# Performance work log

Hardware: AMD Instinct MI355X
Metric: run time of the kernel (lower is better)

Reference implementation:

```python
import jax, jax.numpy as jnp
import numpy as np

N_FFT = 1024
HOP = 256
WIN_LEN = N_FFT  # win_length == n_fft
PAD = (WIN_LEN - HOP) // 2  # 'same' padding


def hann_window(n):
    # torch.hann_window default (periodic=True): 0.5*(1-cos(2*pi*k/n))
    k = jnp.arange(n, dtype=jnp.float32)
    return 0.5 * (1.0 - jnp.cos(2.0 * jnp.pi * k / n))


def setup_inputs() -> dict:
    key = jax.random.key(0)
    k1, k2 = jax.random.split(key)
    B, L, D = 8, 2048, 512
    x = jax.random.normal(k1, (B, L, D), dtype=jnp.float32)
    W = jax.random.normal(k2, (D, N_FFT + 2), dtype=jnp.float32) * (1.0 / np.sqrt(D))
    b = jnp.zeros((N_FFT + 2,), dtype=jnp.float32)
    return {"x": x, "W": W, "b": b}


def reference(x, W, b):
    # Linear projection: (B, L, n_fft+2)
    h = jnp.einsum("bld,do->blo", x, W) + b
    nbins = N_FFT // 2 + 1  # 513
    mag = jnp.minimum(jnp.exp(h[..., :nbins]), 100.0)  # exp + clip max=100
    p = h[..., nbins:]
    # Complex STFT coefficients S: (B, L, nbins)
    S = mag * (jnp.cos(p) + 1j * jnp.sin(p))
    # Per-frame inverse rFFT (norm='backward' = default): (B, L, n_fft)
    frames = jnp.fft.irfft(S, n=N_FFT, axis=-1)
    win = hann_window(WIN_LEN)
    frames = frames * win  # windowed frames
    B, T = frames.shape[0], frames.shape[1]
    out_size = (T - 1) * HOP + WIN_LEN
    # Overlap-add via scatter-add
    idx = jnp.arange(T)[:, None] * HOP + jnp.arange(WIN_LEN)[None, :]  # (T, n_fft)
    y = jnp.zeros((B, out_size), dtype=frames.dtype).at[:, idx].add(frames)
    env = jnp.zeros((out_size,), dtype=frames.dtype).at[idx].add(
        jnp.broadcast_to(win * win, (T, WIN_LEN))
    )
    y = y[:, PAD:-PAD] / env[PAD:-PAD]
    return y
```

## Files before the change

### kernel.cpp

```cpp
#include <hip/hip_runtime.h>
#include <math.h>


using half8 = __attribute__((ext_vector_type(8))) _Float16;
using f32x4 = __attribute__((ext_vector_type(4))) float;

#define TWO_PI_OVER_1024 0.006135923151542565f

#define OFF_A2 0
#define OFF_B2 35651584UL
#define OFF_A1 37879808UL
#define OFF_B1 54657024UL
#define OFF_FL 37879808UL
#define OFF_FH 56754176UL

__device__ __forceinline__ float hannf(int s) {
    return 0.5f * (1.0f - __cosf(TWO_PI_OVER_1024 * (float)s));
}

__device__ __forceinline__ void stage16(const void* g, void* lds) {
    __builtin_amdgcn_global_load_lds(
        (const __attribute__((address_space(1))) void*)g,
        (__attribute__((address_space(3))) void*)lds,
        16, 0, 0);
}

__global__ __launch_bounds__(256)
void prep_k(const float* __restrict__ x, const float* __restrict__ W,
            _Float16* __restrict__ A1, _Float16* __restrict__ B1,
            _Float16* __restrict__ B2)
{
    const int bid = blockIdx.x;
    if (bid < 4096) {
        const size_t tid = (size_t)bid * 256 + threadIdx.x;
        const int l   = (int)(tid & 63);
        const size_t f = tid >> 6;
        const int mts = (int)(f & 7);
        const size_t g = f >> 3;
        const int kt  = (int)(g & 15);
        const int mtb = (int)(g >> 4);
        const int m   = mtb * 128 + mts * 16 + (l & 15);
        const int k0  = kt * 32 + (l >> 4) * 8;
        const float* xp = x + (size_t)m * 512 + k0;
        const float4 v0 = *(const float4*)xp;
        const float4 v1 = *(const float4*)(xp + 4);
        const float vv[8] = {v0.x, v0.y, v0.z, v0.w, v1.x, v1.y, v1.z, v1.w};
        half8 o;
#pragma unroll
        for (int j = 0; j < 8; ++j) o[j] = (_Float16)vv[j];
        *(half8*)(A1 + tid * 8) = o;
    } else if (bid < 4384) {
        const int tid = (bid - 4096) * 256 + threadIdx.x;
        const int l  = tid & 63;
        const int f  = tid >> 6;
        const int t8 = f & 7;
        const int g  = f >> 3;
        const int kt = g & 15;
        const int bx = g >> 4;
        const int side = t8 >> 2;
        const int nt   = t8 & 3;
        const int c    = bx * 64 + nt * 16 + (l & 15);
        const int k0   = kt * 32 + (l >> 4) * 8;
        const int wcol = side ? (513 + c) : c;
        half8 o;
#pragma unroll
        for (int j = 0; j < 8; ++j) {
            float v = (c < 513) ? W[(size_t)(k0 + j) * 1026 + wcol] : 0.0f;
            o[j] = (_Float16)v;
        }
        *(half8*)(B1 + (size_t)tid * 8) = o;
    } else {
        const int tid = (bid - 4384) * 256 + threadIdx.x;
        const int l  = tid & 63;
        const int f  = tid >> 6;
        const int nt = f % 6;
        const int g  = f / 6;
        const int kt = g % 34;
        const int nblk = g / 34;
        const int n  = nblk * 96 + nt * 16 + (l & 15);
        const int kk0 = kt * 32 + (l >> 4) * 8;
        const float win = hannf(n) * (1.0f / 1024.0f);
        half8 o;
#pragma unroll
        for (int j = 0; j < 8; ++j) {
            const int kk = kk0 + j;
            float v = 0.0f;
            if (kk < 544) {
                const int k = kk;
                if (k < 513) {
                    const float coef = (k == 0 || k == 512) ? 1.0f : 2.0f;
                    v = coef * __cosf(TWO_PI_OVER_1024 * (float)((k * n) & 1023)) * win;
                }
            } else {
                const int k = kk - 544;
                if (k < 513) {
                    const float coef = (k == 0 || k == 512) ? 1.0f : 2.0f;
                    v = -coef * __sinf(TWO_PI_OVER_1024 * (float)((k * n) & 1023)) * win;
                }
            }
            o[j] = (_Float16)v;
        }
        *(half8*)(B2 + (size_t)tid * 8) = o;
    }
}


__global__ __launch_bounds__(256, 4)
void gemm1_k(const _Float16* __restrict__ A, const _Float16* __restrict__ B,
             const float* __restrict__ bias, _Float16* __restrict__ A2)
{
    __shared__ _Float16 Ash[2][8 * 512];
    __shared__ _Float16 Bsh[2][8 * 512];
    const int t = threadIdx.x, w = t >> 6, l = t & 63;

    const int lin = blockIdx.x;
    const int xcd = lin & 7, slot = lin >> 3;
    const int mblk = xcd * 16 + slot / 9;
    const int bx   = slot % 9;

    const int wm = (w & 1) * 4;
    const int q  = w >> 1;
    const int jt[4] = {2 * q, 2 * q + 1, 4 + 2 * q, 5 + 2 * q};

    f32x4 acc[4][4];
#pragma unroll
    for (int i = 0; i < 4; ++i)
#pragma unroll
        for (int j = 0; j < 4; ++j) acc[i][j] = (f32x4)0.0f;

    const int lane8 = l * 8;
    const _Float16* Ab = A + ((size_t)mblk * 16 * 8) * 512 + lane8;
    const _Float16* Bb = B + ((size_t)bx * 16 * 8) * 512 + lane8;

    for (int step = 0; step < 8; ++step) {
        const int kt0 = 2 * step;
        __syncthreads();
#pragma unroll
        for (int i = 0; i < 4; ++i) {
            const int s = 4 * w + i;
            const int u = s >> 3, r = s & 7;
            stage16(Ab + ((size_t)(kt0 + u) * 8 + r) * 512, &Ash[u][r * 512]);
            stage16(Bb + ((size_t)(kt0 + u) * 8 + r) * 512, &Bsh[u][r * 512]);
        }
        __syncthreads();

#pragma unroll
        for (int u = 0; u < 2; ++u) {
            half8 a[4], b[4];
#pragma unroll
            for (int i = 0; i < 4; ++i)
                a[i] = *(const half8*)&Ash[u][(wm + i) * 512 + lane8];
#pragma unroll
            for (int j = 0; j < 4; ++j)
                b[j] = *(const half8*)&Bsh[u][jt[j] * 512 + lane8];
#pragma unroll
            for (int i = 0; i < 4; ++i)
#pragma unroll
                for (int j = 0; j < 4; ++j)
                    acc[i][j] = __builtin_amdgcn_mfma_f32_16x16x32_f16(a[i], b[j], acc[i][j], 0, 0, 0);
        }
    }

    _Float16* SrT = &Ash[0][0];
    _Float16* SiT = &Bsh[0][0];

    __syncthreads();
    const int r4 = (l >> 4) * 4, c16 = l & 15;
#pragma unroll
    for (int i = 0; i < 4; ++i) {
        const int row0 = (wm + i) * 16 + r4;
#pragma unroll
        for (int p = 0; p < 2; ++p) {
            const int cl = (2 * q + p) * 16 + c16;
            const int c  = bx * 64 + cl;
            const bool valid = (c < 513);
            const float bm = valid ? bias[c] : 0.0f;
            const float bp = valid ? bias[513 + c] : 0.0f;
#pragma unroll
            for (int r = 0; r < 4; ++r) {
                float Sr = 0.0f, Si = 0.0f;
                if (valid) {
                    const float mag = fminf(__expf(acc[i][p][r] + bm), 100.0f);
                    const float ph  = acc[i][2 + p][r] + bp;
                    Sr = mag * __cosf(ph);
                    Si = mag * __sinf(ph);
                }
                const int row = row0 + r;
                const int idx = row * 64 + (cl ^ ((row & 7) * 8));
                SrT[idx] = (_Float16)Sr;
                SiT[idx] = (_Float16)Si;
            }
        }
    }
    __syncthreads();

#pragma unroll
    for (int f = 0; f < 4; ++f) {
        const int tau  = w * 4 + f;
        const int kt2l = tau >> 3, mts = tau & 7;
        if (bx * 2 + kt2l < 17) {
            const int row = mts * 16 + (l & 15);
            const int kl  = kt2l * 32 + (l >> 4) * 8;
            const int idx = row * 64 + (kl ^ ((row & 7) * 8));
            const half8 vr = *(const half8*)&SrT[idx];
            const half8 vi = *(const half8*)&SiT[idx];
            const int ktr = bx * 2 + kt2l;
            const int kti = 17 + ktr;
            *(half8*)(A2 + ((((size_t)mblk * 34 + ktr) * 8 + mts) * 64 + l) * 8) = vr;
            *(half8*)(A2 + ((((size_t)mblk * 34 + kti) * 8 + mts) * 64 + l) * 8) = vi;
        }
    }
}


__device__ __forceinline__ void mma23(const _Float16* __restrict__ As,
                                      const _Float16* __restrict__ Bs,
                                      int wm, int wn, int lane16, f32x4 (&acc)[2][3])
{
    half8 a[2], b[3];
#pragma unroll
    for (int i = 0; i < 2; ++i) a[i] = *(const half8*)&As[(wm + i) * 512 + lane16];
#pragma unroll
    for (int j = 0; j < 3; ++j) b[j] = *(const half8*)&Bs[(wn + j) * 512 + lane16];
#pragma unroll
    for (int i = 0; i < 2; ++i)
#pragma unroll
        for (int j = 0; j < 3; ++j)
            acc[i][j] = __builtin_amdgcn_mfma_f32_16x16x32_f16(a[i], b[j], acc[i][j], 0, 0, 0);
}

__global__ __launch_bounds__(256, 4)
void gemm2_k(const _Float16* __restrict__ A, const _Float16* __restrict__ Bas,
             _Float16* __restrict__ FL, _Float16* __restrict__ FH)
{
    __shared__ _Float16 SH[10240];
    const int t = threadIdx.x, w = t >> 6, l = t & 63;

    const int lin = blockIdx.x;
    const int xcd = lin & 7, slot = lin >> 3;
    const int mb64 = xcd * 32 + slot / 6;
    const int nblk = slot % 6;
    const int mb128 = mb64 >> 1;
    const int msub  = (mb64 & 1) * 4;

    const int wm = (w & 1) * 2, wn = (w >> 1) * 3;

    f32x4 accC[2][3], accD[2][3];
#pragma unroll
    for (int i = 0; i < 2; ++i)
#pragma unroll
        for (int j = 0; j < 3; ++j) { accC[i][j] = (f32x4)0.0f; accD[i][j] = (f32x4)0.0f; }

    const int lane16 = l * 8;

    for (int step = 0; step < 17; ++step) {
        const int kt0 = 2 * step;
        __syncthreads();
#pragma unroll
        for (int i = 0; i < 5; ++i) {
            const int tau = 5 * w + i;
            if (tau < 8) {
                const int u = tau >> 2, s = tau & 3;
                const _Float16* Ag =
                    A + (((size_t)mb128 * 34 + kt0 + u) * 8 + msub + s) * 512 + lane16;
                stage16(Ag, SH + u * 2048 + s * 512);
            } else {
                const int tb = tau - 8;
                const int u = tb / 6, nt = tb % 6;
                const _Float16* Bg =
                    Bas + (((size_t)nblk * 34 + kt0 + u) * 6 + nt) * 512 + lane16;
                stage16(Bg, SH + 4096 + u * 3072 + nt * 512);
            }
        }
        __syncthreads();

#pragma unroll
        for (int u = 0; u < 2; ++u) {
            const int kt = kt0 + u;
            if (kt < 17) mma23(SH + u * 2048, SH + 4096 + u * 3072, wm, wn, lane16, accC);
            else         mma23(SH + u * 2048, SH + 4096 + u * 3072, wm, wn, lane16, accD);
        }
    }

    const int r4 = (l >> 4) * 4, c0 = l & 15;
    __syncthreads();
#pragma unroll
    for (int i = 0; i < 2; ++i) {
        const int row = (wm + i) * 16 + r4;
#pragma unroll
        for (int j = 0; j < 3; ++j) {
            const int lcol = (wn + j) * 16 + c0;
#pragma unroll
            for (int r = 0; r < 4; ++r)
                SH[(row + r) * 104 + lcol] = (_Float16)(accC[i][j][r] + accD[i][j][r]);
        }
    }
    __syncthreads();
    for (int qq = t; qq < 768; qq += 256) {
        const int row = qq / 12, cc = qq % 12;
        const half8 v = *(const half8*)&SH[row * 104 + cc * 8];
        *(half8*)(FL + (size_t)(mb64 * 64 + row) * 576 + nblk * 96 + cc * 8) = v;
    }
    __syncthreads();

    const int Cbase = (nblk == 5) ? 0 : (416 - 96 * nblk);
    const int lo = (nblk == 5) ? 0 : 1;
    const int hi = (nblk == 0) ? 95 : ((nblk == 5) ? 32 : 96);
#pragma unroll
    for (int i = 0; i < 2; ++i) {
        const int row = (wm + i) * 16 + r4;
#pragma unroll
        for (int j = 0; j < 3; ++j) {
            const int n = nblk * 96 + (wn + j) * 16 + c0;
#pragma unroll
            for (int r = 0; r < 4; ++r) {
                if (n >= 1 && n <= 511)
                    SH[(row + r) * 104 + (512 - n - Cbase)] =
                        (_Float16)(accC[i][j][r] - accD[i][j][r]);
                else if (n == 512)
                    SH[(row + r) * 104 + 0] =
                        (_Float16)(accC[i][j][r] + accD[i][j][r]);
            }
        }
    }
    __syncthreads();
    for (int qq = t; qq < 832; qq += 256) {
        const int row = qq / 13, cc = qq % 13;
        if (8 * cc > hi) continue;
        _Float16* dst = FH + (size_t)(mb64 * 64 + row) * 512 + Cbase + 8 * cc;
        if (8 * cc >= lo && 8 * cc + 7 <= hi) {
            *(half8*)dst = *(const half8*)&SH[row * 104 + cc * 8];
        } else {
#pragma unroll
            for (int e = 0; e < 8; ++e) {
                const int lc = 8 * cc + e;
                if (lc >= lo && lc <= hi) dst[e] = SH[row * 104 + lc];
            }
        }
    }
}


__global__ __launch_bounds__(256)
void ola_kernel(const _Float16* __restrict__ FL, const _Float16* __restrict__ FH,
                float* __restrict__ out)
{
    const int gid = blockIdx.x * 256 + threadIdx.x;
    const size_t base = (size_t)gid * 8;
    const int b  = (int)(base >> 19);
    const int j0 = (int)(base & 524287);
    const int n0 = j0 + 384;

    if (j0 >= 640 && j0 < 523904) {
        const int nb = n0 & 255;
        const int T  = n0 >> 8;
        const size_t mT = (size_t)b * 2048 + T;
        const half8 v0 = *(const half8*)(FL + (mT    ) * 576 + nb);
        const half8 v1 = *(const half8*)(FL + (mT - 1) * 576 + nb + 256);
        const half8 v2 = *(const half8*)(FH + (mT - 2) * 512 + nb);
        const half8 v3 = *(const half8*)(FH + (mT - 3) * 512 + nb + 256);
        f32x4 o0, o1;
#pragma unroll
        for (int e = 0; e < 4; ++e)
            o0[e] = ((float)v0[e] + (float)v1[e] + (float)v2[e] + (float)v3[e]) * (2.0f / 3.0f);
#pragma unroll
        for (int e = 0; e < 4; ++e)
            o1[e] = ((float)v0[4 + e] + (float)v1[4 + e] + (float)v2[4 + e] + (float)v3[4 + e]) * (2.0f / 3.0f);
        *(f32x4*)(out + base) = o0;
        *(f32x4*)(out + base + 4) = o1;
    } else {
        for (int e = 0; e < 8; ++e) {
            const int n = n0 + e;
            int t_hi = n >> 8;
            if (t_hi > 2047) t_hi = 2047;
            const int t_lo = (n >= 1023) ? ((n - 768) >> 8) : 0;
            float acc = 0.0f, env = 0.0f;
            for (int tt = t_lo; tt <= t_hi; ++tt) {
                const int s = n - (tt << 8);
                const float wv = hannf(s);
                const size_t m = (size_t)b * 2048 + tt;
                const float fv = (s < 512) ? (float)FL[m * 576 + s]
                                           : (float)FH[m * 512 + (s - 512)];
                acc += fv;
                env += wv * wv;
            }
            out[base + e] = acc / env;
        }
    }
}


extern "C" void kernel_launch(void* const* d_in, const int* in_sizes, int n_in,
                              void* d_out, int out_size, void* d_ws, size_t ws_size,
                              hipStream_t stream)
{
    const float* x = (const float*)d_in[0];
    const float* W = (const float*)d_in[1];
    const float* b = (const float*)d_in[2];
    float* out = (float*)d_out;
    char* ws = (char*)d_ws;

    _Float16* A2 = (_Float16*)(ws + OFF_A2);
    _Float16* B2 = (_Float16*)(ws + OFF_B2);
    _Float16* A1 = (_Float16*)(ws + OFF_A1);
    _Float16* B1 = (_Float16*)(ws + OFF_B1);
    _Float16* FL = (_Float16*)(ws + OFF_FL);
    _Float16* FH = (_Float16*)(ws + OFF_FH);

    prep_k<<<4690, 256, 0, stream>>>(x, W, A1, B1, B2);

    gemm1_k<<<1152, 256, 0, stream>>>(A1, B1, b, A2);
    gemm2_k<<<1536, 256, 0, stream>>>(A2, B2, FL, FH);

    ola_kernel<<<out_size / 2048, 256, 0, stream>>>(FL, FH, out);
}
```

Baseline: 174.8 us.

## Double-buffer LDS staging in both GEMMs with async prefetch and vmcnt waits

```diff
diff --git a/kernel.cpp b/kernel.cpp
--- a/kernel.cpp
+++ b/kernel.cpp
@@ -24,6 +24,10 @@
         (__attribute__((address_space(3))) void*)lds,
         16, 0, 0);
 }
+
+#define WAITV(N)  asm volatile("s_waitcnt vmcnt(" #N ")" ::: "memory")
+#define BARRIER() asm volatile("s_barrier" ::: "memory")
+#define ENDBAR()  asm volatile("s_waitcnt lgkmcnt(0)\n\ts_barrier" ::: "memory")
 
 __global__ __launch_bounds__(256)
 void prep_k(const float* __restrict__ x, const float* __restrict__ W,
@@ -109,8 +113,7 @@
 void gemm1_k(const _Float16* __restrict__ A, const _Float16* __restrict__ B,
              const float* __restrict__ bias, _Float16* __restrict__ A2)
 {
-    __shared__ _Float16 Ash[2][8 * 512];
-    __shared__ _Float16 Bsh[2][8 * 512];
+    __shared__ _Float16 SH1[16384];
     const int t = threadIdx.x, w = t >> 6, l = t & 63;
 
     const int lin = blockIdx.x;
@@ -129,42 +132,54 @@
         for (int j = 0; j < 4; ++j) acc[i][j] = (f32x4)0.0f;
 
     const int lane8 = l * 8;
-    const _Float16* Ab = A + ((size_t)mblk * 16 * 8) * 512 + lane8;
-    const _Float16* Bb = B + ((size_t)bx * 16 * 8) * 512 + lane8;
-
-    for (int step = 0; step < 8; ++step) {
-        const int kt0 = 2 * step;
-        __syncthreads();
-#pragma unroll
-        for (int i = 0; i < 4; ++i) {
-            const int s = 4 * w + i;
-            const int u = s >> 3, r = s & 7;
-            stage16(Ab + ((size_t)(kt0 + u) * 8 + r) * 512, &Ash[u][r * 512]);
-            stage16(Bb + ((size_t)(kt0 + u) * 8 + r) * 512, &Bsh[u][r * 512]);
-        }
-        __syncthreads();
-
-#pragma unroll
-        for (int u = 0; u < 2; ++u) {
-            half8 a[4], b[4];
-#pragma unroll
-            for (int i = 0; i < 4; ++i)
-                a[i] = *(const half8*)&Ash[u][(wm + i) * 512 + lane8];
+    const _Float16* Ab = A + ((size_t)mblk * 128) * 512 + lane8;
+    const _Float16* Bb = B + ((size_t)bx * 128) * 512 + lane8;
+
+#define G1_STAGE(kt, p)                                                      \
+    {                                                                        \
+        _Pragma("unroll")                                                    \
+        for (int i_ = 0; i_ < 4; ++i_) {                                     \
+            const int tau_ = 4 * w + i_;                                     \
+            if (tau_ < 8)                                                    \
+                stage16(Ab + ((size_t)(kt) * 8 + tau_) * 512,                \
+                        &SH1[(p) * 4096 + tau_ * 512]);                      \
+            else                                                             \
+                stage16(Bb + ((size_t)(kt) * 8 + (tau_ - 8)) * 512,          \
+                        &SH1[8192 + (p) * 4096 + (tau_ - 8) * 512]);         \
+        }                                                                    \
+    }
+
+    G1_STAGE(0, 0);
+    for (int kt = 0; kt < 16; ++kt) {
+        const int p = kt & 1;
+        if (kt < 15) {
+            G1_STAGE(kt + 1, p ^ 1);
+            WAITV(4);
+        } else {
+            WAITV(0);
+        }
+        BARRIER();
+
+        half8 a[4], b[4];
+#pragma unroll
+        for (int i = 0; i < 4; ++i)
+            a[i] = *(const half8*)&SH1[p * 4096 + (wm + i) * 512 + lane8];
+#pragma unroll
+        for (int j = 0; j < 4; ++j)
+            b[j] = *(const half8*)&SH1[8192 + p * 4096 + jt[j] * 512 + lane8];
+#pragma unroll
+        for (int i = 0; i < 4; ++i)
 #pragma unroll
             for (int j = 0; j < 4; ++j)
-                b[j] = *(const half8*)&Bsh[u][jt[j] * 512 + lane8];
-#pragma unroll
-            for (int i = 0; i < 4; ++i)
-#pragma unroll
-                for (int j = 0; j < 4; ++j)
-                    acc[i][j] = __builtin_amdgcn_mfma_f32_16x16x32_f16(a[i], b[j], acc[i][j], 0, 0, 0);
-        }
-    }
-
-    _Float16* SrT = &Ash[0][0];
-    _Float16* SiT = &Bsh[0][0];
-
-    __syncthreads();
+                acc[i][j] = __builtin_amdgcn_mfma_f32_16x16x32_f16(a[i], b[j], acc[i][j], 0, 0, 0);
+
+        ENDBAR();
+    }
+#undef G1_STAGE
+
+    _Float16* SrT = &SH1[0];
+    _Float16* SiT = &SH1[8192];
+
     const int r4 = (l >> 4) * 4, c16 = l & 15;
 #pragma unroll
     for (int i = 0; i < 4; ++i) {
@@ -253,37 +268,41 @@
 
     const int lane16 = l * 8;
 
-    for (int step = 0; step < 17; ++step) {
-        const int kt0 = 2 * step;
-        __syncthreads();
-#pragma unroll
-        for (int i = 0; i < 5; ++i) {
-            const int tau = 5 * w + i;
-            if (tau < 8) {
-                const int u = tau >> 2, s = tau & 3;
-                const _Float16* Ag =
-                    A + (((size_t)mb128 * 34 + kt0 + u) * 8 + msub + s) * 512 + lane16;
-                stage16(Ag, SH + u * 2048 + s * 512);
-            } else {
-                const int tb = tau - 8;
-                const int u = tb / 6, nt = tb % 6;
-                const _Float16* Bg =
-                    Bas + (((size_t)nblk * 34 + kt0 + u) * 6 + nt) * 512 + lane16;
-                stage16(Bg, SH + 4096 + u * 3072 + nt * 512);
-            }
-        }
-        __syncthreads();
-
-#pragma unroll
-        for (int u = 0; u < 2; ++u) {
-            const int kt = kt0 + u;
-            if (kt < 17) mma23(SH + u * 2048, SH + 4096 + u * 3072, wm, wn, lane16, accC);
-            else         mma23(SH + u * 2048, SH + 4096 + u * 3072, wm, wn, lane16, accD);
-        }
-    }
+#define G2_STAGE(kt, p)                                                        \
+    {                                                                          \
+        _Pragma("unroll")                                                      \
+        for (int i_ = 0; i_ < 3; ++i_) {                                       \
+            const int tau_ = w + 4 * i_;                                       \
+            if (tau_ < 4) {                                                    \
+                stage16(A + (((size_t)mb128 * 34 + (kt)) * 8 + msub + tau_) * 512 + lane16, \
+                        &SH[(p) * 5120 + tau_ * 512]);                         \
+            } else if (tau_ < 10) {                                            \
+                const int nt_ = tau_ - 4;                                      \
+                stage16(Bas + (((size_t)nblk * 34 + (kt)) * 6 + nt_) * 512 + lane16, \
+                        &SH[(p) * 5120 + 2048 + nt_ * 512]);                   \
+            }                                                                  \
+        }                                                                      \
+    }
+
+    G2_STAGE(0, 0);
+    for (int kt = 0; kt < 34; ++kt) {
+        const int p = kt & 1;
+        if (kt < 33) {
+            G2_STAGE(kt + 1, p ^ 1);
+            if (w < 2) { WAITV(3); } else { WAITV(2); }
+        } else {
+            WAITV(0);
+        }
+        BARRIER();
+
+        if (kt < 17) mma23(SH + p * 5120, SH + p * 5120 + 2048, wm, wn, lane16, accC);
+        else         mma23(SH + p * 5120, SH + p * 5120 + 2048, wm, wn, lane16, accD);
+
+        ENDBAR();
+    }
+#undef G2_STAGE
 
     const int r4 = (l >> 4) * 4, c0 = l & 15;
-    __syncthreads();
 #pragma unroll
     for (int i = 0; i < 2; ++i) {
         const int row = (wm + i) * 16 + r4;
```

Result: faster. 165.8 us (-5.2%).

## Load GEMM operands directly from global into registers, dropping LDS staging

Applied to the files above, without the earlier changes.

```diff
diff --git a/kernel.cpp b/kernel.cpp
--- a/kernel.cpp
+++ b/kernel.cpp
@@ -16,13 +16,6 @@
 
 __device__ __forceinline__ float hannf(int s) {
     return 0.5f * (1.0f - __cosf(TWO_PI_OVER_1024 * (float)s));
-}
-
-__device__ __forceinline__ void stage16(const void* g, void* lds) {
-    __builtin_amdgcn_global_load_lds(
-        (const __attribute__((address_space(1))) void*)g,
-        (__attribute__((address_space(3))) void*)lds,
-        16, 0, 0);
 }
 
 __global__ __launch_bounds__(256)
@@ -105,12 +98,12 @@
 }
 
 
-__global__ __launch_bounds__(256, 4)
+__global__ __launch_bounds__(256, 3)
 void gemm1_k(const _Float16* __restrict__ A, const _Float16* __restrict__ B,
              const float* __restrict__ bias, _Float16* __restrict__ A2)
 {
-    __shared__ _Float16 Ash[2][8 * 512];
-    __shared__ _Float16 Bsh[2][8 * 512];
+    __shared__ _Float16 SrT[8192];
+    __shared__ _Float16 SiT[8192];
     const int t = threadIdx.x, w = t >> 6, l = t & 63;
 
     const int lin = blockIdx.x;
@@ -132,39 +125,22 @@
     const _Float16* Ab = A + ((size_t)mblk * 16 * 8) * 512 + lane8;
     const _Float16* Bb = B + ((size_t)bx * 16 * 8) * 512 + lane8;
 
-    for (int step = 0; step < 8; ++step) {
-        const int kt0 = 2 * step;
-        __syncthreads();
-#pragma unroll
-        for (int i = 0; i < 4; ++i) {
-            const int s = 4 * w + i;
-            const int u = s >> 3, r = s & 7;
-            stage16(Ab + ((size_t)(kt0 + u) * 8 + r) * 512, &Ash[u][r * 512]);
-            stage16(Bb + ((size_t)(kt0 + u) * 8 + r) * 512, &Bsh[u][r * 512]);
-        }
-        __syncthreads();
-
-#pragma unroll
-        for (int u = 0; u < 2; ++u) {
-            half8 a[4], b[4];
-#pragma unroll
-            for (int i = 0; i < 4; ++i)
-                a[i] = *(const half8*)&Ash[u][(wm + i) * 512 + lane8];
+#pragma unroll 2
+    for (int kt = 0; kt < 16; ++kt) {
+        half8 a[4], b[4];
+#pragma unroll
+        for (int i = 0; i < 4; ++i)
+            a[i] = *(const half8*)(Ab + ((size_t)kt * 8 + wm + i) * 512);
+#pragma unroll
+        for (int j = 0; j < 4; ++j)
+            b[j] = *(const half8*)(Bb + ((size_t)kt * 8 + jt[j]) * 512);
+#pragma unroll
+        for (int i = 0; i < 4; ++i)
 #pragma unroll
             for (int j = 0; j < 4; ++j)
-                b[j] = *(const half8*)&Bsh[u][jt[j] * 512 + lane8];
-#pragma unroll
-            for (int i = 0; i < 4; ++i)
-#pragma unroll
-                for (int j = 0; j < 4; ++j)
-                    acc[i][j] = __builtin_amdgcn_mfma_f32_16x16x32_f16(a[i], b[j], acc[i][j], 0, 0, 0);
-        }
-    }
-
-    _Float16* SrT = &Ash[0][0];
-    _Float16* SiT = &Bsh[0][0];
-
-    __syncthreads();
+                acc[i][j] = __builtin_amdgcn_mfma_f32_16x16x32_f16(a[i], b[j], acc[i][j], 0, 0, 0);
+    }
+
     const int r4 = (l >> 4) * 4, c16 = l & 15;
 #pragma unroll
     for (int i = 0; i < 4; ++i) {
@@ -213,27 +189,11 @@
 }
 
 
-__device__ __forceinline__ void mma23(const _Float16* __restrict__ As,
-                                      const _Float16* __restrict__ Bs,
-                                      int wm, int wn, int lane16, f32x4 (&acc)[2][3])
-{
-    half8 a[2], b[3];
-#pragma unroll
-    for (int i = 0; i < 2; ++i) a[i] = *(const half8*)&As[(wm + i) * 512 + lane16];
-#pragma unroll
-    for (int j = 0; j < 3; ++j) b[j] = *(const half8*)&Bs[(wn + j) * 512 + lane16];
-#pragma unroll
-    for (int i = 0; i < 2; ++i)
-#pragma unroll
-        for (int j = 0; j < 3; ++j)
-            acc[i][j] = __builtin_amdgcn_mfma_f32_16x16x32_f16(a[i], b[j], acc[i][j], 0, 0, 0);
-}
-
 __global__ __launch_bounds__(256, 4)
 void gemm2_k(const _Float16* __restrict__ A, const _Float16* __restrict__ Bas,
              _Float16* __restrict__ FL, _Float16* __restrict__ FH)
 {
-    __shared__ _Float16 SH[10240];
+    __shared__ _Float16 SH[6656];
     const int t = threadIdx.x, w = t >> 6, l = t & 63;
 
     const int lin = blockIdx.x;
@@ -252,38 +212,42 @@
         for (int j = 0; j < 3; ++j) { accC[i][j] = (f32x4)0.0f; accD[i][j] = (f32x4)0.0f; }
 
     const int lane16 = l * 8;
-
-    for (int step = 0; step < 17; ++step) {
-        const int kt0 = 2 * step;
-        __syncthreads();
-#pragma unroll
-        for (int i = 0; i < 5; ++i) {
-            const int tau = 5 * w + i;
-            if (tau < 8) {
-                const int u = tau >> 2, s = tau & 3;
-                const _Float16* Ag =
-                    A + (((size_t)mb128 * 34 + kt0 + u) * 8 + msub + s) * 512 + lane16;
-                stage16(Ag, SH + u * 2048 + s * 512);
-            } else {
-                const int tb = tau - 8;
-                const int u = tb / 6, nt = tb % 6;
-                const _Float16* Bg =
-                    Bas + (((size_t)nblk * 34 + kt0 + u) * 6 + nt) * 512 + lane16;
-                stage16(Bg, SH + 4096 + u * 3072 + nt * 512);
-            }
-        }
-        __syncthreads();
-
-#pragma unroll
-        for (int u = 0; u < 2; ++u) {
-            const int kt = kt0 + u;
-            if (kt < 17) mma23(SH + u * 2048, SH + 4096 + u * 3072, wm, wn, lane16, accC);
-            else         mma23(SH + u * 2048, SH + 4096 + u * 3072, wm, wn, lane16, accD);
-        }
+    const _Float16* Abase = A + (size_t)mb128 * 34 * 8 * 512 + lane16;
+    const _Float16* Bbase = Bas + (size_t)nblk * 34 * 6 * 512 + lane16;
+    const int am = msub + wm;
+
+#pragma unroll 2
+    for (int kt = 0; kt < 17; ++kt) {
+        half8 a[2], b[3];
+#pragma unroll
+        for (int i = 0; i < 2; ++i)
+            a[i] = *(const half8*)(Abase + ((size_t)kt * 8 + am + i) * 512);
+#pragma unroll
+        for (int j = 0; j < 3; ++j)
+            b[j] = *(const half8*)(Bbase + ((size_t)kt * 6 + wn + j) * 512);
+#pragma unroll
+        for (int i = 0; i < 2; ++i)
+#pragma unroll
+            for (int j = 0; j < 3; ++j)
+                accC[i][j] = __builtin_amdgcn_mfma_f32_16x16x32_f16(a[i], b[j], accC[i][j], 0, 0, 0);
+    }
+#pragma unroll 2
+    for (int kt = 17; kt < 34; ++kt) {
+        half8 a[2], b[3];
+#pragma unroll
+        for (int i = 0; i < 2; ++i)
+            a[i] = *(const half8*)(Abase + ((size_t)kt * 8 + am + i) * 512);
+#pragma unroll
+        for (int j = 0; j < 3; ++j)
+            b[j] = *(const half8*)(Bbase + ((size_t)kt * 6 + wn + j) * 512);
+#pragma unroll
+        for (int i = 0; i < 2; ++i)
+#pragma unroll
+            for (int j = 0; j < 3; ++j)
+                accD[i][j] = __builtin_amdgcn_mfma_f32_16x16x32_f16(a[i], b[j], accD[i][j], 0, 0, 0);
     }
 
     const int r4 = (l >> 4) * 4, c0 = l & 15;
-    __syncthreads();
 #pragma unroll
     for (int i = 0; i < 2; ++i) {
         const int row = (wm + i) * 16 + r4;
```

Result: no change. 174.8 us (+0.0%).
